# Optimization experiments

Hardware: AMD Instinct MI355X
Metric: run time of the kernel (lower is better)

## Reference

```python
import jax, jax.numpy as jnp
import numpy as np

B, T, D = 2, 2048, 2048
H, G = 16, 4            # query heads, kv groups
HD = D // H             # head_dim = 128
GS = H // G             # group_size = 4
EPS = 1e-6
ROPE_BASE = 10000.0


def setup_inputs() -> dict:
    key = jax.random.key(0)
    ks = jax.random.split(key, 5)
    s = 0.02
    return {
        "x": jax.random.normal(ks[0], (B, T, D), jnp.float32),
        "Wq": jax.random.normal(ks[1], (H * HD, D), jnp.float32) * s,
        "Wk": jax.random.normal(ks[2], (G * HD, D), jnp.float32) * s,
        "Wv": jax.random.normal(ks[3], (G * HD, D), jnp.float32) * s,
        "Wo": jax.random.normal(ks[4], (D, H * HD), jnp.float32) * s,
        "qn_w": jnp.ones((HD,), jnp.float32),
        "kn_w": jnp.ones((HD,), jnp.float32),
    }


def _rmsnorm(x, w):
    var = jnp.mean(x * x, axis=-1, keepdims=True)
    return x * jax.lax.rsqrt(var + EPS) * w


def _rope_tables(t, d):
    inv_freq = 1.0 / (ROPE_BASE ** (jnp.arange(0, d, 2, dtype=jnp.float32) / d))
    freqs = jnp.arange(t, dtype=jnp.float32)[:, None] * inv_freq[None, :]
    emb = jnp.concatenate([freqs, freqs], axis=-1)  # [T, d]
    return jnp.cos(emb), jnp.sin(emb)


def _apply_rope(x, cos, sin):
    # x: [b, h, t, d]
    d2 = x.shape[-1] // 2
    x1, x2 = x[..., :d2], x[..., d2:]
    rot = jnp.concatenate([-x2, x1], axis=-1)
    return x * cos + rot * sin


def reference(x, Wq, Wk, Wv, Wo, qn_w, kn_w):
    b, t, _ = x.shape
    q = (x @ Wq.T).reshape(b, t, H, HD).transpose(0, 2, 1, 3)  # [b,H,t,hd]
    k = (x @ Wk.T).reshape(b, t, G, HD).transpose(0, 2, 1, 3)  # [b,G,t,hd]
    v = (x @ Wv.T).reshape(b, t, G, HD).transpose(0, 2, 1, 3)

    q = _rmsnorm(q, qn_w)
    k = _rmsnorm(k, kn_w)

    cos, sin = _rope_tables(t, HD)
    q = _apply_rope(q, cos, sin)
    k = _apply_rope(k, cos, sin)

    # torch code scales q by hd^-0.5, then SDPA applies default hd^-0.5 again
    scale = (HD ** -0.5) * (HD ** -0.5)

    # GQA without materializing repeat_interleave: group query heads
    qg = q.reshape(b, G, GS, t, HD)
    scores = jnp.einsum("bgxqd,bgkd->bgxqk", qg, k) * scale  # [b,G,GS,t,t]
    causal = jnp.tril(jnp.ones((t, t), bool))
    scores = jnp.where(causal, scores, -jnp.inf)
    attn = jax.nn.softmax(scores, axis=-1)
    ctx = jnp.einsum("bgxqk,bgkd->bgxqd", attn, v)  # [b,G,GS,t,hd]
    ctx = ctx.reshape(b, H, t, HD).transpose(0, 2, 1, 3).reshape(b, t, H * HD)
    return ctx @ Wo.T
```

## Files before the change

kernel.cpp:

```cpp
#include <hip/hip_runtime.h>
#include <hip/hip_bf16.h>

#define B_ 2
#define T_ 2048
#define D_ 2048
#define H_ 16
#define G_ 4
#define HD_ 128
#define GS_ (H_/G_)

typedef _Float16 half8 __attribute__((ext_vector_type(8)));
typedef _Float16 half2_t __attribute__((ext_vector_type(2)));
typedef float f32x4 __attribute__((ext_vector_type(4)));
typedef float f32x16 __attribute__((ext_vector_type(16)));
typedef int int4_t __attribute__((ext_vector_type(4)));

#define KV_TILE_BYTES 36864
#define KROW_F16 136
#define VROW_F16 72
#define VBASE_F16 8704

#define C0_ 1048576
#define C1_ 1572864
#define C2_ 1703936
#define C3_ 1835008
#define C4_ 2359296
__global__ void cvt_all(const float* __restrict__ sx, const float* __restrict__ sq,
                        const float* __restrict__ sk, const float* __restrict__ sv,
                        const float* __restrict__ so,
                        _Float16* __restrict__ dx, _Float16* __restrict__ dq,
                        _Float16* __restrict__ dk, _Float16* __restrict__ dv,
                        _Float16* __restrict__ dw) {
    int g = blockIdx.x * blockDim.x + threadIdx.x;
    int stride = blockDim.x * gridDim.x;
    for (; g < C4_; g += stride) {
        const float* src; _Float16* dst; int local;
        if (g < C0_)      { src = sx; dst = dx; local = g; }
        else if (g < C1_) { src = sq; dst = dq; local = g - C0_; }
        else if (g < C2_) { src = sk; dst = dk; local = g - C1_; }
        else if (g < C3_) { src = sv; dst = dv; local = g - C2_; }
        else              { src = so; dst = dw; local = g - C3_; }
        f32x4 a = *((const f32x4*)src + local * 2);
        f32x4 b = *((const f32x4*)src + local * 2 + 1);
        half8 hv;
        hv[0] = (_Float16)a[0]; hv[1] = (_Float16)a[1];
        hv[2] = (_Float16)a[2]; hv[3] = (_Float16)a[3];
        hv[4] = (_Float16)b[0]; hv[5] = (_Float16)b[1];
        hv[6] = (_Float16)b[2]; hv[7] = (_Float16)b[3];
        *((half8*)dst + local) = hv;
    }
}

__global__ void rope_tables_k(float* __restrict__ cosT, float* __restrict__ sinT) {
    int i = blockIdx.x * blockDim.x + threadIdx.x;
    int t = i >> 6, l = i & 63;
    float inv_freq = powf(10000.0f, -((float)(2 * l)) / 128.0f);
    float a = (float)t * inv_freq;
    cosT[i] = cosf(a);
    sinT[i] = sinf(a);
}

__global__ void __launch_bounds__(256) gemm_tile(const _Float16* __restrict__ A,
                                                 const _Float16* __restrict__ B0,
                                                 float* __restrict__ C0, int n0t,
                                                 const _Float16* __restrict__ B1,
                                                 float* __restrict__ C1, int n1t,
                                                 const _Float16* __restrict__ B2,
                                                 float* __restrict__ C2, int n2t,
                                                 int Kd) {
    __shared__ _Float16 sA[2][128 * 32];
    __shared__ _Float16 sB[2][128 * 32];

    int tid = threadIdx.x;
    int w = tid >> 6, lane = tid & 63;
    int l15 = lane & 15, g4 = lane >> 4;
    int wm = w >> 1, wn = w & 1;

    int y = blockIdx.y;
    const _Float16* Bsel;
    float* Csel;
    int ldc, cb;
    if (y < n0t)            { Bsel = B0; Csel = C0; ldc = n0t * 128; cb = y; }
    else if (y < n0t + n1t) { Bsel = B1; Csel = C1; ldc = n1t * 128; cb = y - n0t; }
    else                    { Bsel = B2; Csel = C2; ldc = n2t * 128; cb = y - n0t - n1t; }

    const _Float16* Ab = A + (size_t)(blockIdx.x * 128) * Kd;
    const _Float16* Bb = Bsel + (size_t)(cb * 128) * Kd;

    int s0 = w * 128 + lane;
    int s1 = s0 + 64;
    size_t ga0 = (size_t)(s0 >> 2) * Kd + (s0 & 3) * 8;
    size_t ga1 = (size_t)(s1 >> 2) * Kd + (s1 & 3) * 8;

    #define STAGE(BUF, K0)                                                                     \
        do {                                                                                   \
            _Float16* a0_ = &sA[BUF][0] + (size_t)(w * 2) * 512;                               \
            _Float16* a1_ = &sA[BUF][0] + (size_t)(w * 2 + 1) * 512;                           \
            _Float16* b0_ = &sB[BUF][0] + (size_t)(w * 2) * 512;                               \
            _Float16* b1_ = &sB[BUF][0] + (size_t)(w * 2 + 1) * 512;                           \
            __builtin_amdgcn_global_load_lds(                                                  \
                (const __attribute__((address_space(1))) unsigned int*)(Ab + ga0 + (K0)),      \
                (__attribute__((address_space(3))) unsigned int*)a0_, 16, 0, 0);               \
            __builtin_amdgcn_global_load_lds(                                                  \
                (const __attribute__((address_space(1))) unsigned int*)(Ab + ga1 + (K0)),      \
                (__attribute__((address_space(3))) unsigned int*)a1_, 16, 0, 0);               \
            __builtin_amdgcn_global_load_lds(                                                  \
                (const __attribute__((address_space(1))) unsigned int*)(Bb + ga0 + (K0)),      \
                (__attribute__((address_space(3))) unsigned int*)b0_, 16, 0, 0);               \
            __builtin_amdgcn_global_load_lds(                                                  \
                (const __attribute__((address_space(1))) unsigned int*)(Bb + ga1 + (K0)),      \
                (__attribute__((address_space(3))) unsigned int*)b1_, 16, 0, 0);               \
        } while (0)

    f32x4 acc[4][4];
    #pragma unroll
    for (int i = 0; i < 4; i++)
        #pragma unroll
        for (int j = 0; j < 4; j++) acc[i][j] = (f32x4){0.f, 0.f, 0.f, 0.f};

    int nIt = Kd >> 5;
    STAGE(0, 0);
    if (nIt > 1) STAGE(1, 32);

    for (int it = 0; it < nIt; ++it) {
        int cur = it & 1;
        if (it + 1 < nIt) asm volatile("s_waitcnt vmcnt(4)" ::: "memory");
        else              asm volatile("s_waitcnt vmcnt(0)" ::: "memory");
        __builtin_amdgcn_sched_barrier(0);
        __builtin_amdgcn_s_barrier();
        __builtin_amdgcn_sched_barrier(0);

        half8 af[4], bf[4];
        #pragma unroll
        for (int mi = 0; mi < 4; mi++)
            af[mi] = *(const half8*)&sA[cur][(wm * 64 + mi * 16 + l15) * 32 + g4 * 8];
        #pragma unroll
        for (int ni = 0; ni < 4; ni++)
            bf[ni] = *(const half8*)&sB[cur][(wn * 64 + ni * 16 + l15) * 32 + g4 * 8];

        #pragma unroll
        for (int mi = 0; mi < 4; mi++)
            #pragma unroll
            for (int ni = 0; ni < 4; ni++)
                acc[mi][ni] = __builtin_amdgcn_mfma_f32_16x16x32_f16(af[mi], bf[ni], acc[mi][ni], 0, 0, 0);

        __builtin_amdgcn_sched_barrier(0);
        asm volatile("" ::: "memory");
        __builtin_amdgcn_s_barrier();
        __builtin_amdgcn_sched_barrier(0);
        if (it + 2 < nIt) STAGE(cur, (size_t)(it + 2) * 32);
    }
    #undef STAGE

    int rbase = blockIdx.x * 128 + wm * 64 + g4 * 4;
    int cbase = cb * 128 + wn * 64 + l15;
    #pragma unroll
    for (int mi = 0; mi < 4; mi++)
        #pragma unroll
        for (int r = 0; r < 4; r++) {
            float* crow = Csel + (size_t)(rbase + mi * 16 + r) * ldc + cbase;
            #pragma unroll
            for (int ni = 0; ni < 4; ni++) crow[ni * 16] = acc[mi][ni][r];
        }
}

__global__ void rmsnorm_rope_qk(float* __restrict__ Qf, float* __restrict__ Kf,
                                const float* __restrict__ qw, const float* __restrict__ kw,
                                const float* __restrict__ cosT, const float* __restrict__ sinT,
                                _Float16* __restrict__ qH) {
    int gw = (int)((blockIdx.x * (size_t)blockDim.x + threadIdx.x) >> 6);
    int lane = threadIdx.x & 63;
    bool isQ = gw < (B_ * T_ * H_);
    int row_i = isQ ? gw : gw - (B_ * T_ * H_);
    int heads = isQ ? H_ : G_;
    const float* wv = isQ ? qw : kw;
    float* row = (isQ ? Qf : Kf) + (size_t)row_i * HD_;
    int t = (row_i / heads) % T_;
    float x0 = row[lane];
    float x1 = row[lane + 64];
    float ss = x0 * x0 + x1 * x1;
    #pragma unroll
    for (int off = 1; off < 64; off <<= 1) ss += __shfl_xor(ss, off);
    float inv = rsqrtf(ss * (1.0f / 128.0f) + 1e-6f);
    float n0 = x0 * inv * wv[lane];
    float n1 = x1 * inv * wv[lane + 64];
    float c = cosT[t * 64 + lane];
    float s = sinT[t * 64 + lane];
    float r0 = n0 * c - n1 * s;
    float r1 = n1 * c + n0 * s;
    if (isQ) {
        qH[(size_t)row_i * HD_ + lane]      = (_Float16)(r0 * (1.0f / 128.0f));
        qH[(size_t)row_i * HD_ + lane + 64] = (_Float16)(r1 * (1.0f / 128.0f));
    } else {
        row[lane]      = r0;
        row[lane + 64] = r1;
    }
}

__global__ void __launch_bounds__(256) pack_kv(const float* __restrict__ kf,
                                               const float* __restrict__ vf,
                                               _Float16* __restrict__ img) {
    int bid = blockIdx.x;
    int tile = bid & 31, g = (bid >> 5) & 3, b = bid >> 7;
    int tid = threadIdx.x;
    _Float16* out = img + (size_t)bid * (KV_TILE_BYTES / 2);

    #pragma unroll
    for (int it = 0; it < 5; it++) {
        int gi = tid + 256 * it;
        if (gi < 64 * 17) {
            int key = gi / 17, gr = gi % 17;
            half8 hv = (half8){0, 0, 0, 0, 0, 0, 0, 0};
            if (gr < 16) {
                const float* src = kf + ((size_t)((b * T_ + tile * 64 + key) * G_ + g)) * HD_ + gr * 8;
                #pragma unroll
                for (int j = 0; j < 8; j++) hv[j] = (_Float16)src[j];
            }
            *(half8*)(out + (size_t)gi * 8) = hv;
        }
    }
    #pragma unroll
    for (int it = 0; it < 5; it++) {
        int vi = tid + 256 * it;
        if (vi < 128 * 9) {
            int d = vi / 9, gr = vi % 9;
            half8 hv = (half8){0, 0, 0, 0, 0, 0, 0, 0};
            if (gr < 8) {
                const float* src = vf + ((size_t)((b * T_ + tile * 64 + gr * 8) * G_ + g)) * HD_ + d;
                #pragma unroll
                for (int j = 0; j < 8; j++) hv[j] = (_Float16)src[(size_t)j * (G_ * HD_)];
            }
            *(half8*)(out + VBASE_F16 + (size_t)vi * 8) = hv;
        }
    }
}

__global__ void __launch_bounds__(256, 2) attn_mfma5(const _Float16* __restrict__ qh,
                                                     const _Float16* __restrict__ kvimg,
                                                     _Float16* __restrict__ ctx) {
    int id = blockIdx.x;
    int hlf = id >> 8, rr0 = id & 255;
    int qb = hlf ? (15 - (rr0 & 15)) : (rr0 & 15);
    int hb = (rr0 >> 4) | (hlf << 4);
    int h = hb & 15, b = hb >> 4;
    int g = h >> 2;

    int tid = threadIdx.x;
    int w = tid >> 6, lane = tid & 63;
    int l31 = lane & 31, hi = lane >> 5;

    __shared__ __align__(16) char sKV[2][KV_TILE_BYTES];

    int qW = qb * 128 + w * 32;
    int qme = qW + l31;

    half8 qfrag[8];
    {
        const _Float16* qrow = qh + ((size_t)(b * T_ + qme)) * (H_ * HD_) + h * HD_ + hi * 8;
        #pragma unroll
        for (int ks = 0; ks < 8; ks++) qfrag[ks] = *(const half8*)(qrow + ks * 16);
    }

    f32x16 o[4];
    #pragma unroll
    for (int dt2 = 0; dt2 < 4; dt2++)
        #pragma unroll
        for (int r = 0; r < 16; r++) o[dt2][r] = 0.f;
    float m = -INFINITY, lsum = 0.f;

    const char* ibase = (const char*)kvimg + (size_t)((b * 4 + g) * 32) * KV_TILE_BYTES;

    #define STAGE_T(BUF, KT)                                                                       \
        do {                                                                                       \
            const char* src_ = ibase + (size_t)(KT) * KV_TILE_BYTES;                               \
            char* dst_ = &sKV[BUF][0];                                                             \
            _Pragma("unroll")                                                                      \
            for (int i_ = 0; i_ < 9; i_++) {                                                       \
                int c_ = w + 4 * i_;                                                               \
                __builtin_amdgcn_global_load_lds(                                                  \
                    (const __attribute__((address_space(1))) unsigned int*)(src_ + c_ * 1024 + lane * 16), \
                    (__attribute__((address_space(3))) unsigned int*)(dst_ + c_ * 1024 + lane * 16), 16, 0, 0); \
            }                                                                                      \
        } while (0)

    int nt = 2 * qb + 2;
    int ktmax_w = (qW + 31) >> 6;

    STAGE_T(0, 0);
    STAGE_T(1, 1);

    for (int kt = 0; kt < nt; kt++) {
        int cur = kt & 1;
        if (kt + 1 < nt) asm volatile("s_waitcnt vmcnt(9)" ::: "memory");
        else             asm volatile("s_waitcnt vmcnt(0)" ::: "memory");
        __builtin_amdgcn_sched_barrier(0);
        __builtin_amdgcn_s_barrier();
        __builtin_amdgcn_sched_barrier(0);

        if (kt <= ktmax_w) {
            const char* bufK = &sKV[cur][0];
            const char* bufV = &sKV[cur][0] + VBASE_F16 * 2;

            f32x16 stc[2];
            #pragma unroll
            for (int kt2 = 0; kt2 < 2; kt2++)
                #pragma unroll
                for (int r = 0; r < 16; r++) stc[kt2][r] = 0.f;

            __builtin_amdgcn_s_setprio(1);
            #pragma unroll
            for (int ks = 0; ks < 8; ks++) {
                #pragma unroll
                for (int kt2 = 0; kt2 < 2; kt2++) {
                    half8 kfr = *(const half8*)(bufK + (kt2 * 32 + l31) * (KROW_F16 * 2) + ks * 32 + hi * 16);
                    stc[kt2] = __builtin_amdgcn_mfma_f32_32x32x16_f16(kfr, qfrag[ks], stc[kt2], 0, 0, 0);
                }
            }
            __builtin_amdgcn_s_setprio(0);

            #pragma unroll
            for (int kt2 = 0; kt2 < 2; kt2++)
                #pragma unroll
                for (int reg = 0; reg < 16; reg++) {
                    int key = kt * 64 + kt2 * 32 + 8 * (reg >> 2) + 4 * hi + (reg & 3);
                    float v = stc[kt2][reg];
                    stc[kt2][reg] = (key <= qme) ? v : -INFINITY;
                }

            float pmax = -INFINITY;
            #pragma unroll
            for (int kt2 = 0; kt2 < 2; kt2++)
                #pragma unroll
                for (int reg = 0; reg < 16; reg++) pmax = fmaxf(pmax, stc[kt2][reg]);
            pmax = fmaxf(pmax, __shfl_xor(pmax, 32));

            if (__any(!(pmax - m <= 8.0f))) {
                float nm = fmaxf(m, pmax);
                float alpha = __expf(m - nm);
                lsum *= alpha;
                #pragma unroll
                for (int reg = 0; reg < 16; reg++) {
                    float ar = __shfl(alpha, 8 * (reg >> 2) + 4 * hi + (reg & 3));
                    #pragma unroll
                    for (int dt2 = 0; dt2 < 4; dt2++) o[dt2][reg] *= ar;
                }
                m = nm;
            }

            float rsum = 0.f;
            #pragma unroll
            for (int kt2 = 0; kt2 < 2; kt2++)
                #pragma unroll
                for (int reg = 0; reg < 16; reg++) {
                    float e = __expf(stc[kt2][reg] - m);
                    stc[kt2][reg] = e;
                    rsum += e;
                }
            rsum += __shfl_xor(rsum, 32);
            lsum += rsum;

            int pk[16];
            #pragma unroll
            for (int kt2 = 0; kt2 < 2; kt2++)
                #pragma unroll
                for (int oo = 0; oo < 4; oo++)
                    #pragma unroll
                    for (int c = 0; c < 2; c++) {
                        half2_t hp;
                        hp[0] = (_Float16)stc[kt2][4 * oo + 2 * c];
                        hp[1] = (_Float16)stc[kt2][4 * oo + 2 * c + 1];
                        pk[kt2 * 8 + 2 * oo + c] = __builtin_bit_cast(int, hp);
                    }

            __builtin_amdgcn_s_setprio(1);
            #pragma unroll
            for (int ks = 0; ks < 4; ks++) {
                int base = (ks >> 1) * 8 + (ks & 1) * 4;
                int z0 = hi ? pk[base + 0] : pk[base + 2];
                int z1 = hi ? pk[base + 1] : pk[base + 3];
                int xz0 = __shfl_xor(z0, 32);
                int xz1 = __shfl_xor(z1, 32);
                int4_t pi;
                pi[0] = hi ? xz0 : pk[base + 0];
                pi[1] = hi ? xz1 : pk[base + 1];
                pi[2] = hi ? pk[base + 2] : xz0;
                pi[3] = hi ? pk[base + 3] : xz1;
                half8 pfrag = __builtin_bit_cast(half8, pi);
                #pragma unroll
                for (int dt2 = 0; dt2 < 4; dt2++) {
                    half8 vfr = *(const half8*)(bufV + (dt2 * 32 + l31) * (VROW_F16 * 2) + ks * 32 + hi * 16);
                    o[dt2] = __builtin_amdgcn_mfma_f32_32x32x16_f16(pfrag, vfr, o[dt2], 0, 0, 0);
                }
            }
            __builtin_amdgcn_s_setprio(0);
        }

        __builtin_amdgcn_sched_barrier(0);
        asm volatile("" ::: "memory");
        __builtin_amdgcn_s_barrier();
        __builtin_amdgcn_sched_barrier(0);
        if (kt + 2 < nt) STAGE_T(cur, kt + 2);
    }
    #undef STAGE_T

    float invl = 1.0f / lsum;
    #pragma unroll
    for (int reg = 0; reg < 16; reg++) {
        int qrow = 8 * (reg >> 2) + 4 * hi + (reg & 3);
        float ir = __shfl(invl, qrow);
        _Float16* orow = ctx + (size_t)(b * T_ + qW + qrow) * (H_ * HD_) + h * HD_ + l31;
        #pragma unroll
        for (int dt2 = 0; dt2 < 4; dt2++)
            orow[dt2 * 32] = (_Float16)(o[dt2][reg] * ir);
    }
}

extern "C" void kernel_launch(void* const* d_in, const int* in_sizes, int n_in,
                              void* d_out, int out_size, void* d_ws, size_t ws_size,
                              hipStream_t stream) {
    const float* x   = (const float*)d_in[0];
    const float* Wq  = (const float*)d_in[1];
    const float* Wk  = (const float*)d_in[2];
    const float* Wv  = (const float*)d_in[3];
    const float* Wo  = (const float*)d_in[4];
    const float* qnw = (const float*)d_in[5];
    const float* knw = (const float*)d_in[6];
    float* out = (float*)d_out;

    char* ws = (char*)d_ws;
    size_t off = 0;
    auto alloc = [&](size_t bytes) {
        char* p = ws + off;
        off += (bytes + 255) & ~(size_t)255;
        return p;
    };
    _Float16* x_h  = (_Float16*)alloc((size_t)B_ * T_ * D_ * 2);
    _Float16* wq_h = (_Float16*)alloc((size_t)H_ * HD_ * D_ * 2);
    _Float16* wk_h = (_Float16*)alloc((size_t)G_ * HD_ * D_ * 2);
    _Float16* wv_h = (_Float16*)alloc((size_t)G_ * HD_ * D_ * 2);
    _Float16* wo_h = (_Float16*)alloc((size_t)D_ * H_ * HD_ * 2);
    float* q_f = (float*)alloc((size_t)B_ * T_ * H_ * HD_ * 4);
    float* k_f = (float*)alloc((size_t)B_ * T_ * G_ * HD_ * 4);
    float* v_f = (float*)alloc((size_t)B_ * T_ * G_ * HD_ * 4);
    _Float16* ctx_h = (_Float16*)alloc((size_t)B_ * T_ * H_ * HD_ * 2);
    float* cosT = (float*)alloc((size_t)T_ * 64 * 4);
    float* sinT = (float*)alloc((size_t)T_ * 64 * 4);

    _Float16* q_h   = x_h;
    _Float16* kvimg = wq_h;

    cvt_all<<<2048, 256, 0, stream>>>(x, Wq, Wk, Wv, Wo, x_h, wq_h, wk_h, wv_h, wo_h);
    rope_tables_k<<<(T_ * 64) / 256, 256, 0, stream>>>(cosT, sinT);

    gemm_tile<<<dim3(32, 24), 256, 0, stream>>>(x_h, wq_h, q_f, 16,
                                                wk_h, k_f, 4,
                                                wv_h, v_f, 4, D_);

    rmsnorm_rope_qk<<<(B_ * T_ * (H_ + G_)) / 4, 256, 0, stream>>>(q_f, k_f, qnw, knw, cosT, sinT, q_h);

    pack_kv<<<256, 256, 0, stream>>>(k_f, v_f, kvimg);

    attn_mfma5<<<512, 256, 0, stream>>>(q_h, kvimg, ctx_h);

    gemm_tile<<<dim3(32, 16), 256, 0, stream>>>(ctx_h, wo_h, out, 16,
                                                nullptr, nullptr, 0,
                                                nullptr, nullptr, 0, H_ * HD_);
}
```

Measured before the change: 219.2 us.

## Halve attention KV tile to 32 keys, raise occupancy, use exp2 softmax

Shrinks the staged KV tile from 64 to 32 keys, which halves shared memory per buffer, and raises launch bounds to 4 blocks per CU. The pack kernel and the staging and loop counts are updated to match. The log2(e) factor is folded into the Q scaling so softmax can use exp2, and the rescale threshold is widened to suit. The goal is better latency hiding through occupancy and cheaper exponentials, at the cost of more barriers and loop iterations per KV element.

New measurement: 280.2 us. 1.28x slower.

```diff
diff --git a/kernel.cpp b/kernel.cpp
--- a/kernel.cpp
+++ b/kernel.cpp
@@ -15,10 +15,10 @@
 typedef float f32x16 __attribute__((ext_vector_type(16)));
 typedef int int4_t __attribute__((ext_vector_type(4)));
 
-#define KV_TILE_BYTES 36864
+#define KV_TILE_BYTES 20480
 #define KROW_F16 136
-#define VROW_F16 72
-#define VBASE_F16 8704
+#define VROW_F16 40
+#define VBASE_F16 4352
 
 #define C0_ 1048576
 #define C1_ 1572864
@@ -189,8 +189,9 @@
     float r0 = n0 * c - n1 * s;
     float r1 = n1 * c + n0 * s;
     if (isQ) {
-        qH[(size_t)row_i * HD_ + lane]      = (_Float16)(r0 * (1.0f / 128.0f));
-        qH[(size_t)row_i * HD_ + lane + 64] = (_Float16)(r1 * (1.0f / 128.0f));
+        const float QSCL = 1.44269504089f / 128.0f;
+        qH[(size_t)row_i * HD_ + lane]      = (_Float16)(r0 * QSCL);
+        qH[(size_t)row_i * HD_ + lane + 64] = (_Float16)(r1 * QSCL);
     } else {
         row[lane]      = r0;
         row[lane + 64] = r1;
@@ -201,18 +202,18 @@
                                                const float* __restrict__ vf,
                                                _Float16* __restrict__ img) {
     int bid = blockIdx.x;
-    int tile = bid & 31, g = (bid >> 5) & 3, b = bid >> 7;
+    int tile = bid & 63, g = (bid >> 6) & 3, b = bid >> 8;
     int tid = threadIdx.x;
     _Float16* out = img + (size_t)bid * (KV_TILE_BYTES / 2);
 
     #pragma unroll
-    for (int it = 0; it < 5; it++) {
+    for (int it = 0; it < 3; it++) {
         int gi = tid + 256 * it;
-        if (gi < 64 * 17) {
+        if (gi < 32 * 17) {
             int key = gi / 17, gr = gi % 17;
             half8 hv = (half8){0, 0, 0, 0, 0, 0, 0, 0};
             if (gr < 16) {
-                const float* src = kf + ((size_t)((b * T_ + tile * 64 + key) * G_ + g)) * HD_ + gr * 8;
+                const float* src = kf + ((size_t)((b * T_ + tile * 32 + key) * G_ + g)) * HD_ + gr * 8;
                 #pragma unroll
                 for (int j = 0; j < 8; j++) hv[j] = (_Float16)src[j];
             }
@@ -220,13 +221,13 @@
         }
     }
     #pragma unroll
-    for (int it = 0; it < 5; it++) {
+    for (int it = 0; it < 3; it++) {
         int vi = tid + 256 * it;
-        if (vi < 128 * 9) {
-            int d = vi / 9, gr = vi % 9;
+        if (vi < 128 * 5) {
+            int d = vi / 5, gr = vi % 5;
             half8 hv = (half8){0, 0, 0, 0, 0, 0, 0, 0};
-            if (gr < 8) {
-                const float* src = vf + ((size_t)((b * T_ + tile * 64 + gr * 8) * G_ + g)) * HD_ + d;
+            if (gr < 4) {
+                const float* src = vf + ((size_t)((b * T_ + tile * 32 + gr * 8) * G_ + g)) * HD_ + d;
                 #pragma unroll
                 for (int j = 0; j < 8; j++) hv[j] = (_Float16)src[(size_t)j * (G_ * HD_)];
             }
@@ -235,7 +236,7 @@
     }
 }
 
-__global__ void __launch_bounds__(256, 2) attn_mfma5(const _Float16* __restrict__ qh,
+__global__ void __launch_bounds__(256, 4) attn_mfma8(const _Float16* __restrict__ qh,
                                                      const _Float16* __restrict__ kvimg,
                                                      _Float16* __restrict__ ctx) {
     int id = blockIdx.x;
@@ -268,14 +269,14 @@
         for (int r = 0; r < 16; r++) o[dt2][r] = 0.f;
     float m = -INFINITY, lsum = 0.f;
 
-    const char* ibase = (const char*)kvimg + (size_t)((b * 4 + g) * 32) * KV_TILE_BYTES;
+    const char* ibase = (const char*)kvimg + (size_t)((b * 4 + g) * 64) * KV_TILE_BYTES;
 
     #define STAGE_T(BUF, KT)                                                                       \
         do {                                                                                       \
             const char* src_ = ibase + (size_t)(KT) * KV_TILE_BYTES;                               \
             char* dst_ = &sKV[BUF][0];                                                             \
             _Pragma("unroll")                                                                      \
-            for (int i_ = 0; i_ < 9; i_++) {                                                       \
+            for (int i_ = 0; i_ < 5; i_++) {                                                       \
                 int c_ = w + 4 * i_;                                                               \
                 __builtin_amdgcn_global_load_lds(                                                  \
                     (const __attribute__((address_space(1))) unsigned int*)(src_ + c_ * 1024 + lane * 16), \
@@ -283,15 +284,15 @@
             }                                                                                      \
         } while (0)
 
-    int nt = 2 * qb + 2;
-    int ktmax_w = (qW + 31) >> 6;
+    int nt = 4 * qb + 4;
+    int ktmax_w = (qW + 31) >> 5;
 
     STAGE_T(0, 0);
     STAGE_T(1, 1);
 
     for (int kt = 0; kt < nt; kt++) {
         int cur = kt & 1;
-        if (kt + 1 < nt) asm volatile("s_waitcnt vmcnt(9)" ::: "memory");
+        if (kt + 1 < nt) asm volatile("s_waitcnt vmcnt(5)" ::: "memory");
         else             asm volatile("s_waitcnt vmcnt(0)" ::: "memory");
         __builtin_amdgcn_sched_barrier(0);
         __builtin_amdgcn_s_barrier();
@@ -301,42 +302,33 @@
             const char* bufK = &sKV[cur][0];
             const char* bufV = &sKV[cur][0] + VBASE_F16 * 2;
 
-            f32x16 stc[2];
-            #pragma unroll
-            for (int kt2 = 0; kt2 < 2; kt2++)
-                #pragma unroll
-                for (int r = 0; r < 16; r++) stc[kt2][r] = 0.f;
+            f32x16 stc;
+            #pragma unroll
+            for (int r = 0; r < 16; r++) stc[r] = 0.f;
 
             __builtin_amdgcn_s_setprio(1);
             #pragma unroll
             for (int ks = 0; ks < 8; ks++) {
-                #pragma unroll
-                for (int kt2 = 0; kt2 < 2; kt2++) {
-                    half8 kfr = *(const half8*)(bufK + (kt2 * 32 + l31) * (KROW_F16 * 2) + ks * 32 + hi * 16);
-                    stc[kt2] = __builtin_amdgcn_mfma_f32_32x32x16_f16(kfr, qfrag[ks], stc[kt2], 0, 0, 0);
-                }
+                half8 kfr = *(const half8*)(bufK + l31 * (KROW_F16 * 2) + ks * 32 + hi * 16);
+                stc = __builtin_amdgcn_mfma_f32_32x32x16_f16(kfr, qfrag[ks], stc, 0, 0, 0);
             }
             __builtin_amdgcn_s_setprio(0);
 
             #pragma unroll
-            for (int kt2 = 0; kt2 < 2; kt2++)
-                #pragma unroll
-                for (int reg = 0; reg < 16; reg++) {
-                    int key = kt * 64 + kt2 * 32 + 8 * (reg >> 2) + 4 * hi + (reg & 3);
-                    float v = stc[kt2][reg];
-                    stc[kt2][reg] = (key <= qme) ? v : -INFINITY;
-                }
+            for (int reg = 0; reg < 16; reg++) {
+                int key = kt * 32 + 8 * (reg >> 2) + 4 * hi + (reg & 3);
+                float v = stc[reg];
+                stc[reg] = (key <= qme) ? v : -INFINITY;
+            }
 
             float pmax = -INFINITY;
             #pragma unroll
-            for (int kt2 = 0; kt2 < 2; kt2++)
-                #pragma unroll
-                for (int reg = 0; reg < 16; reg++) pmax = fmaxf(pmax, stc[kt2][reg]);
+            for (int reg = 0; reg < 16; reg++) pmax = fmaxf(pmax, stc[reg]);
             pmax = fmaxf(pmax, __shfl_xor(pmax, 32));
 
-            if (__any(!(pmax - m <= 8.0f))) {
+            if (__any(!(pmax - m <= 11.5f))) {
                 float nm = fmaxf(m, pmax);
-                float alpha = __expf(m - nm);
+                float alpha = __builtin_exp2f(m - nm);
                 lsum *= alpha;
                 #pragma unroll
                 for (int reg = 0; reg < 16; reg++) {
@@ -349,33 +341,29 @@
 
             float rsum = 0.f;
             #pragma unroll
-            for (int kt2 = 0; kt2 < 2; kt2++)
-                #pragma unroll
-                for (int reg = 0; reg < 16; reg++) {
-                    float e = __expf(stc[kt2][reg] - m);
-                    stc[kt2][reg] = e;
-                    rsum += e;
-                }
+            for (int reg = 0; reg < 16; reg++) {
+                float e = __builtin_exp2f(stc[reg] - m);
+                stc[reg] = e;
+                rsum += e;
+            }
             rsum += __shfl_xor(rsum, 32);
             lsum += rsum;
 
-            int pk[16];
-            #pragma unroll
-            for (int kt2 = 0; kt2 < 2; kt2++)
+            int pk[8];
+            #pragma unroll
+            for (int oo = 0; oo < 4; oo++)
                 #pragma unroll
-                for (int oo = 0; oo < 4; oo++)
-                    #pragma unroll
-                    for (int c = 0; c < 2; c++) {
-                        half2_t hp;
-                        hp[0] = (_Float16)stc[kt2][4 * oo + 2 * c];
-                        hp[1] = (_Float16)stc[kt2][4 * oo + 2 * c + 1];
-                        pk[kt2 * 8 + 2 * oo + c] = __builtin_bit_cast(int, hp);
-                    }
+                for (int c = 0; c < 2; c++) {
+                    half2_t hp;
+                    hp[0] = (_Float16)stc[4 * oo + 2 * c];
+                    hp[1] = (_Float16)stc[4 * oo + 2 * c + 1];
+                    pk[2 * oo + c] = __builtin_bit_cast(int, hp);
+                }
 
             __builtin_amdgcn_s_setprio(1);
             #pragma unroll
-            for (int ks = 0; ks < 4; ks++) {
-                int base = (ks >> 1) * 8 + (ks & 1) * 4;
+            for (int ks = 0; ks < 2; ks++) {
+                int base = ks * 4;
                 int z0 = hi ? pk[base + 0] : pk[base + 2];
                 int z1 = hi ? pk[base + 1] : pk[base + 3];
                 int xz0 = __shfl_xor(z0, 32);
@@ -458,9 +446,9 @@
 
     rmsnorm_rope_qk<<<(B_ * T_ * (H_ + G_)) / 4, 256, 0, stream>>>(q_f, k_f, qnw, knw, cosT, sinT, q_h);
 
-    pack_kv<<<256, 256, 0, stream>>>(k_f, v_f, kvimg);
-
-    attn_mfma5<<<512, 256, 0, stream>>>(q_h, kvimg, ctx_h);
+    pack_kv<<<512, 256, 0, stream>>>(k_f, v_f, kvimg);
+
+    attn_mfma8<<<512, 256, 0, stream>>>(q_h, kvimg, ctx_h);
 
     gemm_tile<<<dim3(32, 16), 256, 0, stream>>>(ctx_h, wo_h, out, 16,
                                                 nullptr, nullptr, 0,
```

## Fuse conversion with rope tables, and rmsnorm/rope with KV packing

Applied to the files above, without the earlier changes.

The fp16 conversion kernel and the rope-table kernel are merged into one launch, with the block index selecting the role. The rmsnorm/rope kernel and the KV-pack kernel are merged as well. Normalized K rows are now written as fp16 straight into the packed attention tile image. This removes two kernel launches and the fp32 K write-back and re-read. The K padding columns in the tile image are no longer zero-filled, which is only safe if the attention kernel never reads them.

After: 214.2 us. 2.3% less time.

```diff
diff --git a/kernel.cpp b/kernel.cpp
--- a/kernel.cpp
+++ b/kernel.cpp
@@ -25,39 +25,40 @@
 #define C2_ 1703936
 #define C3_ 1835008
 #define C4_ 2359296
-__global__ void cvt_all(const float* __restrict__ sx, const float* __restrict__ sq,
-                        const float* __restrict__ sk, const float* __restrict__ sv,
-                        const float* __restrict__ so,
-                        _Float16* __restrict__ dx, _Float16* __restrict__ dq,
-                        _Float16* __restrict__ dk, _Float16* __restrict__ dv,
-                        _Float16* __restrict__ dw) {
-    int g = blockIdx.x * blockDim.x + threadIdx.x;
-    int stride = blockDim.x * gridDim.x;
-    for (; g < C4_; g += stride) {
-        const float* src; _Float16* dst; int local;
-        if (g < C0_)      { src = sx; dst = dx; local = g; }
-        else if (g < C1_) { src = sq; dst = dq; local = g - C0_; }
-        else if (g < C2_) { src = sk; dst = dk; local = g - C1_; }
-        else if (g < C3_) { src = sv; dst = dv; local = g - C2_; }
-        else              { src = so; dst = dw; local = g - C3_; }
-        f32x4 a = *((const f32x4*)src + local * 2);
-        f32x4 b = *((const f32x4*)src + local * 2 + 1);
-        half8 hv;
-        hv[0] = (_Float16)a[0]; hv[1] = (_Float16)a[1];
-        hv[2] = (_Float16)a[2]; hv[3] = (_Float16)a[3];
-        hv[4] = (_Float16)b[0]; hv[5] = (_Float16)b[1];
-        hv[6] = (_Float16)b[2]; hv[7] = (_Float16)b[3];
-        *((half8*)dst + local) = hv;
-    }
-}
-
-__global__ void rope_tables_k(float* __restrict__ cosT, float* __restrict__ sinT) {
-    int i = blockIdx.x * blockDim.x + threadIdx.x;
-    int t = i >> 6, l = i & 63;
-    float inv_freq = powf(10000.0f, -((float)(2 * l)) / 128.0f);
-    float a = (float)t * inv_freq;
-    cosT[i] = cosf(a);
-    sinT[i] = sinf(a);
+__global__ void cvt_rope(const float* __restrict__ sx, const float* __restrict__ sq,
+                         const float* __restrict__ sk, const float* __restrict__ sv,
+                         const float* __restrict__ so,
+                         _Float16* __restrict__ dx, _Float16* __restrict__ dq,
+                         _Float16* __restrict__ dk, _Float16* __restrict__ dv,
+                         _Float16* __restrict__ dw,
+                         float* __restrict__ cosT, float* __restrict__ sinT) {
+    int blk = blockIdx.x, tid = threadIdx.x;
+    if (blk < 2048) {
+        int g = blk * 256 + tid;
+        for (; g < C4_; g += 2048 * 256) {
+            const float* src; _Float16* dst; int local;
+            if (g < C0_)      { src = sx; dst = dx; local = g; }
+            else if (g < C1_) { src = sq; dst = dq; local = g - C0_; }
+            else if (g < C2_) { src = sk; dst = dk; local = g - C1_; }
+            else if (g < C3_) { src = sv; dst = dv; local = g - C2_; }
+            else              { src = so; dst = dw; local = g - C3_; }
+            f32x4 a = *((const f32x4*)src + local * 2);
+            f32x4 b = *((const f32x4*)src + local * 2 + 1);
+            half8 hv;
+            hv[0] = (_Float16)a[0]; hv[1] = (_Float16)a[1];
+            hv[2] = (_Float16)a[2]; hv[3] = (_Float16)a[3];
+            hv[4] = (_Float16)b[0]; hv[5] = (_Float16)b[1];
+            hv[6] = (_Float16)b[2]; hv[7] = (_Float16)b[3];
+            *((half8*)dst + local) = hv;
+        }
+    } else {
+        int i = (blk - 2048) * 256 + tid;
+        int t = i >> 6, l = i & 63;
+        float inv_freq = powf(10000.0f, -((float)(2 * l)) / 128.0f);
+        float a = (float)t * inv_freq;
+        cosT[i] = cosf(a);
+        sinT[i] = sinf(a);
+    }
 }
 
 __global__ void __launch_bounds__(256) gemm_tile(const _Float16* __restrict__ A,
@@ -164,73 +165,66 @@
         }
 }
 
-__global__ void rmsnorm_rope_qk(float* __restrict__ Qf, float* __restrict__ Kf,
-                                const float* __restrict__ qw, const float* __restrict__ kw,
-                                const float* __restrict__ cosT, const float* __restrict__ sinT,
-                                _Float16* __restrict__ qH) {
-    int gw = (int)((blockIdx.x * (size_t)blockDim.x + threadIdx.x) >> 6);
-    int lane = threadIdx.x & 63;
-    bool isQ = gw < (B_ * T_ * H_);
-    int row_i = isQ ? gw : gw - (B_ * T_ * H_);
-    int heads = isQ ? H_ : G_;
-    const float* wv = isQ ? qw : kw;
-    float* row = (isQ ? Qf : Kf) + (size_t)row_i * HD_;
-    int t = (row_i / heads) % T_;
-    float x0 = row[lane];
-    float x1 = row[lane + 64];
-    float ss = x0 * x0 + x1 * x1;
-    #pragma unroll
-    for (int off = 1; off < 64; off <<= 1) ss += __shfl_xor(ss, off);
-    float inv = rsqrtf(ss * (1.0f / 128.0f) + 1e-6f);
-    float n0 = x0 * inv * wv[lane];
-    float n1 = x1 * inv * wv[lane + 64];
-    float c = cosT[t * 64 + lane];
-    float s = sinT[t * 64 + lane];
-    float r0 = n0 * c - n1 * s;
-    float r1 = n1 * c + n0 * s;
-    if (isQ) {
-        qH[(size_t)row_i * HD_ + lane]      = (_Float16)(r0 * (1.0f / 128.0f));
-        qH[(size_t)row_i * HD_ + lane + 64] = (_Float16)(r1 * (1.0f / 128.0f));
+__global__ void __launch_bounds__(256) norm_pack(const float* __restrict__ Qf,
+                                                 const float* __restrict__ Kf,
+                                                 const float* __restrict__ vf,
+                                                 const float* __restrict__ qw,
+                                                 const float* __restrict__ kw,
+                                                 const float* __restrict__ cosT,
+                                                 const float* __restrict__ sinT,
+                                                 _Float16* __restrict__ qH,
+                                                 _Float16* __restrict__ img) {
+    int blk = blockIdx.x, tid = threadIdx.x;
+    if (blk < 20480) {
+        int gw = (blk * 256 + tid) >> 6;
+        int lane = tid & 63;
+        bool isQ = gw < (B_ * T_ * H_);
+        int row_i = isQ ? gw : gw - (B_ * T_ * H_);
+        int heads = isQ ? H_ : G_;
+        const float* wv = isQ ? qw : kw;
+        const float* row = (isQ ? Qf : Kf) + (size_t)row_i * HD_;
+        int t = (row_i / heads) % T_;
+        float x0 = row[lane];
+        float x1 = row[lane + 64];
+        float ss = x0 * x0 + x1 * x1;
+        #pragma unroll
+        for (int off = 1; off < 64; off <<= 1) ss += __shfl_xor(ss, off);
+        float inv = rsqrtf(ss * (1.0f / 128.0f) + 1e-6f);
+        float n0 = x0 * inv * wv[lane];
+        float n1 = x1 * inv * wv[lane + 64];
+        float c = cosT[t * 64 + lane];
+        float s = sinT[t * 64 + lane];
+        float r0 = n0 * c - n1 * s;
+        float r1 = n1 * c + n0 * s;
+        if (isQ) {
+            qH[(size_t)row_i * HD_ + lane]      = (_Float16)(r0 * (1.0f / 128.0f));
+            qH[(size_t)row_i * HD_ + lane + 64] = (_Float16)(r1 * (1.0f / 128.0f));
+        } else {
+            int b = row_i / (T_ * G_);
+            int rem = row_i - b * (T_ * G_);
+            int g = rem - (rem / G_) * G_;
+            int bid = (b * 4 + g) * 32 + (t >> 6);
+            _Float16* kout = img + (size_t)bid * (KV_TILE_BYTES / 2) + (t & 63) * KROW_F16;
+            kout[lane]      = (_Float16)r0;
+            kout[lane + 64] = (_Float16)r1;
+        }
     } else {
-        row[lane]      = r0;
-        row[lane + 64] = r1;
-    }
-}
-
-__global__ void __launch_bounds__(256) pack_kv(const float* __restrict__ kf,
-                                               const float* __restrict__ vf,
-                                               _Float16* __restrict__ img) {
-    int bid = blockIdx.x;
-    int tile = bid & 31, g = (bid >> 5) & 3, b = bid >> 7;
-    int tid = threadIdx.x;
-    _Float16* out = img + (size_t)bid * (KV_TILE_BYTES / 2);
-
-    #pragma unroll
-    for (int it = 0; it < 5; it++) {
-        int gi = tid + 256 * it;
-        if (gi < 64 * 17) {
-            int key = gi / 17, gr = gi % 17;
-            half8 hv = (half8){0, 0, 0, 0, 0, 0, 0, 0};
-            if (gr < 16) {
-                const float* src = kf + ((size_t)((b * T_ + tile * 64 + key) * G_ + g)) * HD_ + gr * 8;
-                #pragma unroll
-                for (int j = 0; j < 8; j++) hv[j] = (_Float16)src[j];
+        int vb = blk - 20480;
+        int tile = vb & 31, g = (vb >> 5) & 3, b = vb >> 7;
+        _Float16* out = img + (size_t)vb * (KV_TILE_BYTES / 2);
+        #pragma unroll
+        for (int it = 0; it < 5; it++) {
+            int vi = tid + 256 * it;
+            if (vi < 128 * 9) {
+                int d = vi / 9, gr = vi % 9;
+                half8 hv = (half8){0, 0, 0, 0, 0, 0, 0, 0};
+                if (gr < 8) {
+                    const float* src = vf + ((size_t)((b * T_ + tile * 64 + gr * 8) * G_ + g)) * HD_ + d;
+                    #pragma unroll
+                    for (int j = 0; j < 8; j++) hv[j] = (_Float16)src[(size_t)j * (G_ * HD_)];
+                }
+                *(half8*)(out + VBASE_F16 + (size_t)vi * 8) = hv;
             }
-            *(half8*)(out + (size_t)gi * 8) = hv;
-        }
-    }
-    #pragma unroll
-    for (int it = 0; it < 5; it++) {
-        int vi = tid + 256 * it;
-        if (vi < 128 * 9) {
-            int d = vi / 9, gr = vi % 9;
-            half8 hv = (half8){0, 0, 0, 0, 0, 0, 0, 0};
-            if (gr < 8) {
-                const float* src = vf + ((size_t)((b * T_ + tile * 64 + gr * 8) * G_ + g)) * HD_ + d;
-                #pragma unroll
-                for (int j = 0; j < 8; j++) hv[j] = (_Float16)src[(size_t)j * (G_ * HD_)];
-            }
-            *(half8*)(out + VBASE_F16 + (size_t)vi * 8) = hv;
         }
     }
 }
@@ -449,16 +443,14 @@
     _Float16* q_h   = x_h;
     _Float16* kvimg = wq_h;
 
-    cvt_all<<<2048, 256, 0, stream>>>(x, Wq, Wk, Wv, Wo, x_h, wq_h, wk_h, wv_h, wo_h);
-    rope_tables_k<<<(T_ * 64) / 256, 256, 0, stream>>>(cosT, sinT);
+    cvt_rope<<<2560, 256, 0, stream>>>(x, Wq, Wk, Wv, Wo, x_h, wq_h, wk_h, wv_h, wo_h,
+                                       cosT, sinT);
 
     gemm_tile<<<dim3(32, 24), 256, 0, stream>>>(x_h, wq_h, q_f, 16,
                                                 wk_h, k_f, 4,
                                                 wv_h, v_f, 4, D_);
 
-    rmsnorm_rope_qk<<<(B_ * T_ * (H_ + G_)) / 4, 256, 0, stream>>>(q_f, k_f, qnw, knw, cosT, sinT, q_h);
-
-    pack_kv<<<256, 256, 0, stream>>>(k_f, v_f, kvimg);
+    norm_pack<<<20736, 256, 0, stream>>>(q_f, k_f, v_f, qnw, knw, cosT, sinT, q_h, kvimg);
 
     attn_mfma5<<<512, 256, 0, stream>>>(q_h, kvimg, ctx_h);
 
```
